# Performance work log

Measured on AMD Instinct MI355X. Metric: run time of the kernel, lower is better.

Reference implementation:

```python
import jax, jax.numpy as jnp
import numpy as np

TAU = 0.9
TOPK = 8
NUM_LAYERS = 3


def _layer_norm(x, g, b, eps=1e-5):
    mu = jnp.mean(x, axis=-1, keepdims=True)
    var = jnp.var(x, axis=-1, keepdims=True)
    return (x - mu) / jnp.sqrt(var + eps) * g + b


def _forward(x, edge_index, Wi, bi, wp, Wa, ba, ln1_g, ln1_b, ln2_g, ln2_b,
             W1, b1, W2, b2, Wc, bc, Wo, bo):
    N = x.shape[0]
    H = Wi.shape[1]
    # input projection + relu
    x = jax.nn.relu(x @ Wi + bi)
    src, dst = edge_index[0], edge_index[1]
    # ---- priority pi (computed under no_grad, dummy_alpha = 1, x_prev = 0) ----
    delta_x = jnp.sum(jnp.abs(x), axis=1)                      # [N]
    neigh = jax.ops.segment_sum(delta_x[src], dst, num_segments=N)
    pi = jax.lax.stop_gradient(jax.nn.sigmoid(x @ wp + neigh))  # [N]
    # ---- add self loops (selected subgraph == full graph) ----
    loops = jnp.arange(N, dtype=src.dtype)
    src_e = jnp.concatenate([src, loops])
    dst_e = jnp.concatenate([dst, loops])
    Et = src_e.shape[0]
    # ---- edge attention logits: att_mlp(cat[h_i, h_j, p_j]) computed as split matvec ----
    a_dst = x @ Wa[:H]          # contribution of h_i = x[dst]
    a_src = x @ Wa[H:2 * H]     # contribution of h_j = x[src]
    e = a_dst[dst_e] + a_src[src_e] + pi[src_e] * Wa[2 * H] + ba[0]
    e = jax.nn.leaky_relu(e, 0.2) / TAU
    e = jnp.clip(e, -5.0, 5.0)
    exp_e = jnp.exp(e)
    denom = jax.ops.segment_sum(exp_e, dst_e, num_segments=N)
    alpha = exp_e / (denom[dst_e] + 1e-16)
    # ---- per-destination top-k sparsification + renormalization (vectorized) ----
    order = jnp.lexsort((-alpha, dst_e))       # sort by dst, then alpha descending
    dst_s = dst_e[order]
    alpha_s = alpha[order]
    pos = jnp.arange(Et)
    is_new = jnp.concatenate([jnp.ones((1,), bool), dst_s[1:] != dst_s[:-1]])
    grp_start = jax.lax.cummax(jnp.where(is_new, pos, 0))
    rank = pos - grp_start                     # rank within each dst group
    keep = rank < TOPK
    ksum = jax.ops.segment_sum(jnp.where(keep, alpha_s, 0.0), dst_s, num_segments=N)
    alpha_new_s = jnp.where(keep, alpha_s / (ksum[dst_s] + 1e-16), 0.0)
    alpha = jnp.zeros((Et,), x.dtype).at[order].set(alpha_new_s)
    # ---- prenorm blocks with priority-weighted conv (dropout = identity, eval) ----
    h = x
    for l in range(NUM_LAYERS):
        hn = _layer_norm(h, ln1_g[l], ln1_b[l])
        xp = hn @ Wc[l] + bc[l]                               # conv linear
        msg = xp[src_e] * alpha[:, None]                      # [Et, H]
        agg = jax.ops.segment_sum(msg, dst_e, num_segments=N)  # scatter-add
        h = h + jax.nn.relu(agg)
        h2 = _layer_norm(h, ln2_g[l], ln2_b[l])
        h2 = jax.nn.gelu(h2 @ W1[l] + b1[l], approximate=False) @ W2[l] + b2[l]
        h = h + h2
    return h @ Wo + bo


def setup_inputs() -> dict:
    key = jax.random.key(0)
    ks = jax.random.split(key, 10)
    N, E, IN, H, OUT, L, F = 50000, 400000, 256, 256, 64, 3, 512
    def nrm(k, shape, scale):
        return jax.random.normal(k, shape, jnp.float32) * scale
    return {
        "x": nrm(ks[0], (N, IN), 1.0),
        "edge_index": jax.random.randint(ks[1], (2, E), 0, N, dtype=jnp.int32),
        "Wi": nrm(ks[2], (IN, H), IN ** -0.5), "bi": jnp.zeros((H,), jnp.float32),
        "wp": nrm(ks[3], (H,), H ** -0.5),
        "Wa": nrm(ks[4], (2 * H + 1,), (2 * H + 1) ** -0.5), "ba": jnp.zeros((1,), jnp.float32),
        "ln1_g": jnp.ones((L, H), jnp.float32), "ln1_b": jnp.zeros((L, H), jnp.float32),
        "ln2_g": jnp.ones((L, H), jnp.float32), "ln2_b": jnp.zeros((L, H), jnp.float32),
        "W1": nrm(ks[5], (L, H, F), H ** -0.5), "b1": jnp.zeros((L, F), jnp.float32),
        "W2": nrm(ks[6], (L, F, H), F ** -0.5), "b2": jnp.zeros((L, H), jnp.float32),
        "Wc": nrm(ks[7], (L, H, H), H ** -0.5), "bc": jnp.zeros((L, H), jnp.float32),
        "Wo": nrm(ks[8], (H, OUT), H ** -0.5), "bo": jnp.zeros((OUT,), jnp.float32),
    }


def reference(x, edge_index, Wi, bi, wp, Wa, ba, ln1_g, ln1_b, ln2_g, ln2_b,
              W1, b1, W2, b2, Wc, bc, Wo, bo):
    return _forward(x, edge_index, Wi, bi, wp, Wa, ba, ln1_g, ln1_b, ln2_g, ln2_b,
                    W1, b1, W2, b2, Wc, bc, Wo, bo)
```

## Files before the change

### kernel.cpp

```cpp
#include <hip/hip_runtime.h>
#include <math.h>

#define TAUF 0.9f

typedef unsigned int u32;
typedef unsigned short ushort;
typedef __attribute__((ext_vector_type(8))) short short8;
typedef __attribute__((ext_vector_type(8))) _Float16 half8;
typedef __attribute__((ext_vector_type(4))) _Float16 half4;
typedef __attribute__((ext_vector_type(4))) float f32x4;
typedef __attribute__((ext_vector_type(4))) unsigned short us4;

__device__ __forceinline__ float wave_sum(float v) {
#pragma unroll
  for (int off = 32; off > 0; off >>= 1) v += __shfl_down(v, off, 64);
  return __shfl(v, 0, 64);
}

__device__ __forceinline__ ushort f2bf(float f) {
  u32 u = __builtin_bit_cast(u32, f);
  u32 r = (u + 0x7FFFu + ((u >> 16) & 1u)) >> 16;
  return (ushort)r;
}
__device__ __forceinline__ float bf2f(ushort s) {
  u32 u = ((u32)s) << 16;
  return __builtin_bit_cast(float, u);
}

__device__ __forceinline__ void gload16(const void* g, void* l) {
  __builtin_amdgcn_global_load_lds(
      (const __attribute__((address_space(1))) u32*)g,
      (__attribute__((address_space(3))) u32*)l, 16, 0, 0);
}

__launch_bounds__(256, 2)
__global__ void gemm_in_mfma(const _Float16* __restrict__ Ah, const _Float16* __restrict__ Al,
                             const _Float16* __restrict__ Bh, const _Float16* __restrict__ Bl,
                             const float* __restrict__ bias, const float* __restrict__ Wa,
                             const float* __restrict__ wp, const float* __restrict__ g1,
                             const float* __restrict__ b1g, float* __restrict__ C,
                             ushort* __restrict__ hn, float* __restrict__ delta,
                             float* __restrict__ adst, float* __restrict__ asrc,
                             float* __restrict__ xwp, int M) {
  __shared__ char lds[81920];
  char* As_h = lds;
  char* As_l = lds + 8192;
  char* Bs_h = lds + 16384;
  char* Bs_l = lds + 49152;
  const int tid = threadIdx.x;
  const int wave = tid >> 6, lane = tid & 63;
  const int bm = blockIdx.x * 64;
  const int srow = lane >> 3;
  const int scol = (((lane & 7) ^ srow) << 3);

  f32x4 accH[4][4], accC[4][4];
#pragma unroll
  for (int i = 0; i < 4; ++i)
#pragma unroll
    for (int j = 0; j < 4; ++j) {
      accH[i][j] = (f32x4){0.f, 0.f, 0.f, 0.f};
      accC[i][j] = (f32x4){0.f, 0.f, 0.f, 0.f};
    }

  for (int k0 = 0; k0 < 256; k0 += 64) {
#pragma unroll
    for (int r = 0; r < 2; ++r) {
      const int ch = r * 4 + wave;
      int ar = bm + ch * 8 + srow;
      ar = (ar < M) ? ar : (M - 1);
      gload16(Ah + (size_t)ar * 256 + k0 + scol, As_h + ch * 1024);
      gload16(Al + (size_t)ar * 256 + k0 + scol, As_l + ch * 1024);
    }
#pragma unroll
    for (int r = 0; r < 8; ++r) {
      const int ch = r * 4 + wave;
      const int br = ch * 8 + srow;
      gload16(Bh + (size_t)br * 256 + k0 + scol, Bs_h + ch * 1024);
      gload16(Bl + (size_t)br * 256 + k0 + scol, Bs_l + ch * 1024);
    }
    __syncthreads();
#pragma unroll
    for (int kk = 0; kk < 2; ++kk) {
      const int c = (kk * 32 + (lane >> 4) * 8) * 2;
      half8 ah[4], bh[4];
#pragma unroll
      for (int mi = 0; mi < 4; ++mi) {
        const int rr = mi * 16 + (lane & 15);
        ah[mi] = *(const half8*)(As_h + rr * 128 + (c ^ ((rr & 7) << 4)));
      }
#pragma unroll
      for (int ni = 0; ni < 4; ++ni) {
        const int rr = wave * 64 + ni * 16 + (lane & 15);
        bh[ni] = *(const half8*)(Bs_h + rr * 128 + (c ^ ((rr & 7) << 4)));
      }
#pragma unroll
      for (int mi = 0; mi < 4; ++mi)
#pragma unroll
        for (int ni = 0; ni < 4; ++ni)
          accH[mi][ni] = __builtin_amdgcn_mfma_f32_16x16x32_f16(ah[mi], bh[ni],
                                                                accH[mi][ni], 0, 0, 0);
      half8 al[4];
#pragma unroll
      for (int mi = 0; mi < 4; ++mi) {
        const int rr = mi * 16 + (lane & 15);
        al[mi] = *(const half8*)(As_l + rr * 128 + (c ^ ((rr & 7) << 4)));
      }
#pragma unroll
      for (int mi = 0; mi < 4; ++mi)
#pragma unroll
        for (int ni = 0; ni < 4; ++ni)
          accC[mi][ni] = __builtin_amdgcn_mfma_f32_16x16x32_f16(al[mi], bh[ni],
                                                                accC[mi][ni], 0, 0, 0);
      half8 bl[4];
#pragma unroll
      for (int ni = 0; ni < 4; ++ni) {
        const int rr = wave * 64 + ni * 16 + (lane & 15);
        bl[ni] = *(const half8*)(Bs_l + rr * 128 + (c ^ ((rr & 7) << 4)));
      }
#pragma unroll
      for (int mi = 0; mi < 4; ++mi)
#pragma unroll
        for (int ni = 0; ni < 4; ++ni)
          accC[mi][ni] = __builtin_amdgcn_mfma_f32_16x16x32_f16(ah[mi], bl[ni],
                                                                accC[mi][ni], 0, 0, 0);
    }
    __syncthreads();
  }

  float bb[4], wa0[4], wa1[4], wpv[4], gg[4], gb[4];
#pragma unroll
  for (int ni = 0; ni < 4; ++ni) {
    const int c = wave * 64 + ni * 16 + (lane & 15);
    bb[ni] = bias[c]; wa0[ni] = Wa[c]; wa1[ni] = Wa[256 + c];
    wpv[ni] = wp[c]; gg[ni] = g1[c]; gb[ni] = b1g[c];
  }
  float* red = (float*)lds;
  float* muA = (float*)(lds + 5120);
  float* isA = (float*)(lds + 5376);
  const float inv = 1.f / 2048.f;
#pragma unroll
  for (int mi = 0; mi < 4; ++mi) {
#pragma unroll
    for (int reg = 0; reg < 4; ++reg) {
      const int lrow = mi * 16 + (lane >> 4) * 4 + reg;
      const int row = bm + lrow;
      float v[4];
      float p0 = 0.f, p1 = 0.f, p2 = 0.f, p3 = 0.f, p4 = 0.f;
#pragma unroll
      for (int ni = 0; ni < 4; ++ni) {
        float t = accH[mi][ni][reg] + accC[mi][ni][reg] * inv + bb[ni];
        t = fmaxf(t, 0.f);
        v[ni] = t;
        p0 += t; p1 += t * wa0[ni]; p2 += t * wa1[ni]; p3 += t * wpv[ni];
        p4 += t * t;
      }
      if (row < M) {
#pragma unroll
        for (int ni = 0; ni < 4; ++ni)
          C[(size_t)row * 256 + wave * 64 + ni * 16 + (lane & 15)] = v[ni];
      }
#pragma unroll
      for (int ni = 0; ni < 4; ++ni) accH[mi][ni][reg] = v[ni];
#pragma unroll
      for (int off = 1; off < 16; off <<= 1) {
        p0 += __shfl_xor(p0, off, 64);
        p1 += __shfl_xor(p1, off, 64);
        p2 += __shfl_xor(p2, off, 64);
        p3 += __shfl_xor(p3, off, 64);
        p4 += __shfl_xor(p4, off, 64);
      }
      if ((lane & 15) == 0) {
        red[(0 * 4 + wave) * 64 + lrow] = p0;
        red[(1 * 4 + wave) * 64 + lrow] = p1;
        red[(2 * 4 + wave) * 64 + lrow] = p2;
        red[(3 * 4 + wave) * 64 + lrow] = p3;
        red[(4 * 4 + wave) * 64 + lrow] = p4;
      }
    }
  }
  __syncthreads();
  if (tid < 64) {
    float s0 = 0.f, s1 = 0.f, s2 = 0.f, s3 = 0.f, s4 = 0.f;
#pragma unroll
    for (int w = 0; w < 4; ++w) {
      s0 += red[(0 * 4 + w) * 64 + tid];
      s1 += red[(1 * 4 + w) * 64 + tid];
      s2 += red[(2 * 4 + w) * 64 + tid];
      s3 += red[(3 * 4 + w) * 64 + tid];
      s4 += red[(4 * 4 + w) * 64 + tid];
    }
    const int row = bm + tid;
    if (row < M) {
      delta[row] = s0; adst[row] = s1; asrc[row] = s2; xwp[row] = s3;
    }
    float mu = s0 * (1.f / 256.f);
    muA[tid] = mu;
    isA[tid] = rsqrtf(s4 * (1.f / 256.f) - mu * mu + 1e-5f);
  }
  __syncthreads();
#pragma unroll
  for (int mi = 0; mi < 4; ++mi) {
#pragma unroll
    for (int reg = 0; reg < 4; ++reg) {
      const int lrow = mi * 16 + (lane >> 4) * 4 + reg;
      const int row = bm + lrow;
      if (row >= M) continue;
      const float mu = muA[lrow], is = isA[lrow];
#pragma unroll
      for (int ni = 0; ni < 4; ++ni) {
        const int col = wave * 64 + ni * 16 + (lane & 15);
        hn[(size_t)row * 256 + col] = f2bf((accH[mi][ni][reg] - mu) * is * gg[ni] + gb[ni]);
      }
    }
  }
}

__global__ void xsplit_k(const float* __restrict__ X, _Float16* __restrict__ Xh,
                         _Float16* __restrict__ Xl, int total4) {
  int i = blockIdx.x * 256 + threadIdx.x;
  if (i >= total4) return;
  float4 x = reinterpret_cast<const float4*>(X)[i];
  half4 h, l;
  float xs[4] = {x.x, x.y, x.z, x.w};
#pragma unroll
  for (int j = 0; j < 4; ++j) {
    _Float16 hv = (_Float16)xs[j];
    h[j] = hv;
    l[j] = (_Float16)((xs[j] - (float)hv) * 2048.f);
  }
  reinterpret_cast<half4*>(Xh)[i] = h;
  reinterpret_cast<half4*>(Xl)[i] = l;
}

template <int EPI>
__launch_bounds__(256)
__global__ void gemm_mfma(const ushort* __restrict__ A, const ushort* __restrict__ Bt,
                          const float* __restrict__ bias, float* __restrict__ Cf,
                          ushort* __restrict__ Cb, int M, int N, int K) {
  __shared__ ushort As[128 * 64];
  __shared__ ushort Bs[128 * 64];
  const int tid = threadIdx.x;
  const int wave = tid >> 6, lane = tid & 63;
  const int bm = blockIdx.x * 128, bn = blockIdx.y * 128;
  const int wm = (wave >> 1) * 64, wn = (wave & 1) * 64;
  const int srow = lane >> 3;
  const int scol = (((lane & 7) ^ srow) << 3);

  f32x4 acc[4][4];
#pragma unroll
  for (int i = 0; i < 4; ++i)
#pragma unroll
    for (int j = 0; j < 4; ++j) acc[i][j] = (f32x4){0.f, 0.f, 0.f, 0.f};

  for (int k0 = 0; k0 < K; k0 += 64) {
#pragma unroll
    for (int r = 0; r < 4; ++r) {
      const int ch = r * 4 + wave;
      int ar = bm + ch * 8 + srow;
      ar = (ar < M) ? ar : (M - 1);
      gload16(A + (size_t)ar * K + k0 + scol, (char*)As + ch * 1024);
      const int br = bn + ch * 8 + srow;
      gload16(Bt + (size_t)br * K + k0 + scol, (char*)Bs + ch * 1024);
    }
    __syncthreads();
#pragma unroll
    for (int kk = 0; kk < 2; ++kk) {
      const int c = (kk * 32 + (lane >> 4) * 8) * 2;
      short8 a[4];
#pragma unroll
      for (int mi = 0; mi < 4; ++mi) {
        const int rr = wm + mi * 16 + (lane & 15);
        a[mi] = *(const short8*)((const char*)As + rr * 128 + (c ^ ((rr & 7) << 4)));
      }
#pragma unroll
      for (int ni = 0; ni < 4; ++ni) {
        const int rr = wn + ni * 16 + (lane & 15);
        short8 b = *(const short8*)((const char*)Bs + rr * 128 + (c ^ ((rr & 7) << 4)));
#pragma unroll
        for (int mi = 0; mi < 4; ++mi)
          acc[mi][ni] = __builtin_amdgcn_mfma_f32_16x16x32_bf16(a[mi], b,
                                                                acc[mi][ni], 0, 0, 0);
      }
    }
    __syncthreads();
  }

  float bb[4];
#pragma unroll
  for (int ni = 0; ni < 4; ++ni) bb[ni] = bias[bn + wn + ni * 16 + (lane & 15)];
#pragma unroll
  for (int mi = 0; mi < 4; ++mi) {
#pragma unroll
    for (int reg = 0; reg < 4; ++reg) {
      const int row = bm + wm + mi * 16 + (lane >> 4) * 4 + reg;
      if (row >= M) continue;
#pragma unroll
      for (int ni = 0; ni < 4; ++ni) {
        const int col = bn + wn + ni * 16 + (lane & 15);
        float v = acc[mi][ni][reg] + bb[ni];
        if (EPI == 1) {
          Cb[(size_t)row * N + col] = f2bf(v);
        } else if (EPI == 2) {
          v = v * 0.5f * (1.f + erff(v * 0.70710678118654752f));
          Cb[(size_t)row * N + col] = f2bf(v);
        } else if (EPI == 3) {
          Cf[(size_t)row * N + col] += v;
        } else {
          v += Cf[(size_t)row * N + col];
          Cb[(size_t)row * N + col] = f2bf(v);
        }
      }
    }
  }
}

__launch_bounds__(256)
__global__ void gemm_out(const ushort* __restrict__ A, const ushort* __restrict__ Bt,
                         const float* __restrict__ bias, float* __restrict__ C, int M) {
  __shared__ ushort As[128 * 64];
  __shared__ ushort Bs[64 * 64];
  const int tid = threadIdx.x;
  const int wave = tid >> 6, lane = tid & 63;
  const int bm = blockIdx.x * 128;
  const int wm = wave * 32;
  const int srow = lane >> 3;
  const int scol = (((lane & 7) ^ srow) << 3);
  f32x4 acc[2][4];
#pragma unroll
  for (int i = 0; i < 2; ++i)
#pragma unroll
    for (int j = 0; j < 4; ++j) acc[i][j] = (f32x4){0.f, 0.f, 0.f, 0.f};

  for (int k0 = 0; k0 < 256; k0 += 64) {
#pragma unroll
    for (int r = 0; r < 4; ++r) {
      const int ch = r * 4 + wave;
      int ar = bm + ch * 8 + srow;
      ar = (ar < M) ? ar : (M - 1);
      gload16(A + (size_t)ar * 256 + k0 + scol, (char*)As + ch * 1024);
    }
#pragma unroll
    for (int r = 0; r < 2; ++r) {
      const int ch = r * 4 + wave;
      const int br = ch * 8 + srow;
      gload16(Bt + (size_t)br * 256 + k0 + scol, (char*)Bs + ch * 1024);
    }
    __syncthreads();
#pragma unroll
    for (int kk = 0; kk < 2; ++kk) {
      const int c = (kk * 32 + (lane >> 4) * 8) * 2;
      short8 a[2], b[4];
#pragma unroll
      for (int mi = 0; mi < 2; ++mi) {
        const int rr = wm + mi * 16 + (lane & 15);
        a[mi] = *(const short8*)((const char*)As + rr * 128 + (c ^ ((rr & 7) << 4)));
      }
#pragma unroll
      for (int ni = 0; ni < 4; ++ni) {
        const int rr = ni * 16 + (lane & 15);
        b[ni] = *(const short8*)((const char*)Bs + rr * 128 + (c ^ ((rr & 7) << 4)));
      }
#pragma unroll
      for (int mi = 0; mi < 2; ++mi)
#pragma unroll
        for (int ni = 0; ni < 4; ++ni)
          acc[mi][ni] = __builtin_amdgcn_mfma_f32_16x16x32_bf16(a[mi], b[ni],
                                                                acc[mi][ni], 0, 0, 0);
    }
    __syncthreads();
  }
  float bb[4];
#pragma unroll
  for (int ni = 0; ni < 4; ++ni) bb[ni] = bias[ni * 16 + (lane & 15)];
#pragma unroll
  for (int mi = 0; mi < 2; ++mi) {
#pragma unroll
    for (int reg = 0; reg < 4; ++reg) {
      const int row = bm + wm + mi * 16 + (lane >> 4) * 4 + reg;
      if (row >= M) continue;
#pragma unroll
      for (int ni = 0; ni < 4; ++ni) {
        const int col = ni * 16 + (lane & 15);
        C[(size_t)row * 64 + col] = acc[mi][ni][reg] + bb[ni];
      }
    }
  }
}

#define W_IN 65536
#define W_TOTAL (196608 + 393216 + 393216 + 16384)
__global__ void prep_k(const float* __restrict__ Wi, const float* __restrict__ Wc,
                       const float* __restrict__ W1, const float* __restrict__ W2,
                       const float* __restrict__ Wo, _Float16* __restrict__ WiTh,
                       _Float16* __restrict__ WiTl, ushort* __restrict__ WcT,
                       ushort* __restrict__ W1T, ushort* __restrict__ W2T,
                       ushort* __restrict__ WoT, float* __restrict__ zbase, int zn) {
  int i = blockIdx.x * 256 + threadIdx.x;
  if (i < W_IN) {
    int n = i >> 8, k = i & 255;
    float w = Wi[(size_t)k * 256 + n];
    _Float16 hv = (_Float16)w;
    WiTh[i] = hv;
    WiTl[i] = (_Float16)((w - (float)hv) * 2048.f);
  } else if ((i -= W_IN) < W_TOTAL) {
    int j = i;
    if (j < 196608) {
      int l = j / 65536, r = j % 65536, n = r >> 8, k = r & 255;
      WcT[j] = f2bf(Wc[(size_t)l * 65536 + k * 256 + n]);
    } else if ((j -= 196608) < 393216) {
      int l = j / 131072, r = j % 131072, n = r >> 8, k = r & 255;
      W1T[j] = f2bf(W1[(size_t)l * 131072 + k * 512 + n]);
    } else if ((j -= 393216) < 393216) {
      int l = j / 131072, r = j % 131072, n = r >> 9, k = r & 511;
      W2T[j] = f2bf(W2[(size_t)l * 131072 + k * 256 + n]);
    } else {
      j -= 393216;
      int n = j >> 8, k = j & 255;
      WoT[j] = f2bf(Wo[k * 64 + n]);
    }
  } else {
    int z = i - W_TOTAL;
    if (z < zn) zbase[z] = 0.f;
  }
}

__global__ void neigh_k(const int* __restrict__ src, const int* __restrict__ dst,
                        const float* __restrict__ delta, float* __restrict__ neigh, int E) {
  int e = blockIdx.x * 256 + threadIdx.x;
  if (e < E) atomicAdd(&neigh[dst[e]], delta[src[e]]);
}

__global__ void logits_k(const int* __restrict__ src, const int* __restrict__ dst,
                         const float* __restrict__ adst, const float* __restrict__ asrc,
                         const float* __restrict__ xwp, const float* __restrict__ neigh,
                         const float* __restrict__ Wa, const float* __restrict__ ba,
                         float* __restrict__ expe, float* __restrict__ denom,
                         int* __restrict__ cnt, int* __restrict__ slots,
                         int E, int Et, int N) {
  int e = blockIdx.x * 256 + threadIdx.x;
  if (e >= Et) return;
  int s, d;
  if (e < E) { s = src[e]; d = dst[e]; } else { s = e - E; d = s; }
  float pis = 1.f / (1.f + expf(-(xwp[s] + neigh[s])));
  float v = adst[d] + asrc[s] + pis * Wa[512] + ba[0];
  v = (v >= 0.f ? v : 0.2f * v) / TAUF;
  v = fminf(fmaxf(v, -5.f), 5.f);
  float ex = expf(v);
  expe[e] = ex;
  atomicAdd(&denom[d], ex);
  int p = atomicAdd(&cnt[d], 1);
  if (p < 64) slots[(size_t)p * N + d] = e;
}

__device__ __forceinline__ bool better(float a, int e, float a2, int e2) {
  return a > a2 || (a == a2 && e < e2);
}

__global__ void topk_k(const int* __restrict__ cnt, const int* __restrict__ slots,
                       const float* __restrict__ expe, const float* __restrict__ denom,
                       const int* __restrict__ src, int* __restrict__ kcnt,
                       int* __restrict__ ksrc, float* __restrict__ kw, int N, int E) {
  int d = blockIdx.x * 256 + threadIdx.x;
  if (d >= N) return;
  int deg = min(cnt[d], 64);
  float D = denom[d] + 1e-16f;
  float av[8]; int ai[8]; int kc = 0;
  for (int t = 0; t < deg; ++t) {
    int e = slots[(size_t)t * N + d];
    float a = expe[e] / D;
    if (kc < 8) {
      int p = kc++;
      while (p > 0 && better(a, e, av[p - 1], ai[p - 1])) {
        av[p] = av[p - 1]; ai[p] = ai[p - 1]; --p;
      }
      av[p] = a; ai[p] = e;
    } else if (better(a, e, av[7], ai[7])) {
      int p = 7;
      while (p > 0 && better(a, e, av[p - 1], ai[p - 1])) {
        av[p] = av[p - 1]; ai[p] = ai[p - 1]; --p;
      }
      av[p] = a; ai[p] = e;
    }
  }
  float ks = 0.f;
  for (int j = 0; j < kc; ++j) ks += av[j];
  kcnt[d] = kc;
  for (int j = 0; j < kc; ++j) {
    int e = ai[j];
    ksrc[(size_t)d * 8 + j] = (e < E) ? src[e] : (e - E);
    kw[(size_t)d * 8 + j] = av[j] / (ks + 1e-16f);
  }
}

__global__ void ln_k(const float* __restrict__ h, const float* __restrict__ g,
                     const float* __restrict__ b, ushort* __restrict__ o, int N) {
  int row = blockIdx.x * 4 + (threadIdx.x >> 6);
  if (row >= N) return;
  int lane = threadIdx.x & 63;
  float4 v = *reinterpret_cast<const float4*>(h + (size_t)row * 256 + lane * 4);
  float s = wave_sum(v.x + v.y + v.z + v.w);
  float mu = s * (1.f / 256.f);
  float q = (v.x - mu) * (v.x - mu) + (v.y - mu) * (v.y - mu) +
            (v.z - mu) * (v.z - mu) + (v.w - mu) * (v.w - mu);
  q = wave_sum(q);
  float is = rsqrtf(q * (1.f / 256.f) + 1e-5f);
  float4 gg = *reinterpret_cast<const float4*>(g + lane * 4);
  float4 bb = *reinterpret_cast<const float4*>(b + lane * 4);
  us4 out;
  out.x = f2bf((v.x - mu) * is * gg.x + bb.x);
  out.y = f2bf((v.y - mu) * is * gg.y + bb.y);
  out.z = f2bf((v.z - mu) * is * gg.z + bb.z);
  out.w = f2bf((v.w - mu) * is * gg.w + bb.w);
  *reinterpret_cast<us4*>(o + (size_t)row * 256 + lane * 4) = out;
}

__global__ void agg_ln_k(const ushort* __restrict__ xp, const int* __restrict__ kcnt,
                         const int* __restrict__ ksrc, const float* __restrict__ kw,
                         const float* __restrict__ g, const float* __restrict__ b,
                         float* __restrict__ h, ushort* __restrict__ hn, int N) {
  int d = blockIdx.x * 4 + (threadIdx.x >> 6);
  if (d >= N) return;
  int lane = threadIdx.x & 63;
  int kc = kcnt[d];
  float a0 = 0.f, a1 = 0.f, a2 = 0.f, a3 = 0.f;
  for (int j = 0; j < kc; ++j) {
    int s = ksrc[(size_t)d * 8 + j];
    float w = kw[(size_t)d * 8 + j];
    us4 xv = *reinterpret_cast<const us4*>(xp + (size_t)s * 256 + lane * 4);
    a0 += w * bf2f(xv.x);
    a1 += w * bf2f(xv.y);
    a2 += w * bf2f(xv.z);
    a3 += w * bf2f(xv.w);
  }
  float* hr = h + (size_t)d * 256 + lane * 4;
  float4 hv = *reinterpret_cast<const float4*>(hr);
  float v0 = hv.x + fmaxf(a0, 0.f);
  float v1 = hv.y + fmaxf(a1, 0.f);
  float v2 = hv.z + fmaxf(a2, 0.f);
  float v3 = hv.w + fmaxf(a3, 0.f);
  *reinterpret_cast<float4*>(hr) = make_float4(v0, v1, v2, v3);
  float s = wave_sum(v0 + v1 + v2 + v3);
  float mu = s * (1.f / 256.f);
  float q = (v0 - mu) * (v0 - mu) + (v1 - mu) * (v1 - mu) +
            (v2 - mu) * (v2 - mu) + (v3 - mu) * (v3 - mu);
  q = wave_sum(q);
  float is = rsqrtf(q * (1.f / 256.f) + 1e-5f);
  float4 gg = *reinterpret_cast<const float4*>(g + lane * 4);
  float4 bb = *reinterpret_cast<const float4*>(b + lane * 4);
  us4 out;
  out.x = f2bf((v0 - mu) * is * gg.x + bb.x);
  out.y = f2bf((v1 - mu) * is * gg.y + bb.y);
  out.z = f2bf((v2 - mu) * is * gg.z + bb.z);
  out.w = f2bf((v3 - mu) * is * gg.w + bb.w);
  *reinterpret_cast<us4*>(hn + (size_t)d * 256 + lane * 4) = out;
}

extern "C" void kernel_launch(void* const* d_in, const int* in_sizes, int n_in,
                              void* d_out, int out_size, void* d_ws, size_t ws_size,
                              hipStream_t stream) {
  const float* X   = (const float*)d_in[0];
  const int*   EI  = (const int*)d_in[1];
  const float* Wi  = (const float*)d_in[2];
  const float* bi  = (const float*)d_in[3];
  const float* wp  = (const float*)d_in[4];
  const float* Wa  = (const float*)d_in[5];
  const float* ba  = (const float*)d_in[6];
  const float* l1g = (const float*)d_in[7];
  const float* l1b = (const float*)d_in[8];
  const float* l2g = (const float*)d_in[9];
  const float* l2b = (const float*)d_in[10];
  const float* W1  = (const float*)d_in[11];
  const float* b1  = (const float*)d_in[12];
  const float* W2  = (const float*)d_in[13];
  const float* b2  = (const float*)d_in[14];
  const float* Wc  = (const float*)d_in[15];
  const float* bc  = (const float*)d_in[16];
  const float* Wo  = (const float*)d_in[17];
  const float* bo  = (const float*)d_in[18];

  const int N = in_sizes[0] / 256;
  const int E = in_sizes[1] / 2;
  const int Et = E + N;
  const int* srcp = EI;
  const int* dstp = EI + E;

  float* ws = (float*)d_ws;
  size_t off = 0;
  auto alloc = [&](size_t n) { float* p = ws + off; off += n; return p; };
  const size_t NH = (size_t)N * 256;
  float*  h    = alloc(NH);
  ushort* hn   = (ushort*)alloc(NH / 2);
  ushort* xp   = (ushort*)alloc(NH / 2);
  float*  ualias = alloc(NH);
  ushort* u    = (ushort*)ualias;
  _Float16* Xh = (_Float16*)ualias;
  _Float16* Xl = Xh + NH;
  _Float16* WiTh = (_Float16*)alloc(65536 / 2);
  _Float16* WiTl = (_Float16*)alloc(65536 / 2);
  ushort* WcT  = (ushort*)alloc(3 * 65536 / 2);
  ushort* W1T  = (ushort*)alloc(3 * 131072 / 2);
  ushort* W2T  = (ushort*)alloc(3 * 131072 / 2);
  ushort* WoT  = (ushort*)alloc(16384 / 2);
  float* delta = alloc(N);
  float* adst  = alloc(N);
  float* asrc  = alloc(N);
  float* xwp   = alloc(N);
  float* expe  = alloc(Et);
  float* neigh = alloc(N);
  float* denom = alloc(N);
  int*   cnt   = (int*)alloc(N);
  int*   slots = (int*)alloc((size_t)N * 64);
  int*   kcnt  = (int*)alloc(N);
  int*   ksrc  = (int*)alloc((size_t)N * 8);
  float* kw    = alloc((size_t)N * 8);

  prep_k<<<(W_IN + W_TOTAL + 3 * N + 255) / 256, 256, 0, stream>>>(
      Wi, Wc, W1, W2, Wo, WiTh, WiTl, WcT, W1T, W2T, WoT, neigh, 3 * N);
  xsplit_k<<<((int)(NH / 4) + 255) / 256, 256, 0, stream>>>(X, Xh, Xl, (int)(NH / 4));

  gemm_in_mfma<<<(N + 63) / 64, 256, 0, stream>>>(
      Xh, Xl, WiTh, WiTl, bi, Wa, wp, l1g, l1b, h, hn,
      delta, adst, asrc, xwp, N);
  neigh_k<<<(E + 255) / 256, 256, 0, stream>>>(srcp, dstp, delta, neigh, E);
  logits_k<<<(Et + 255) / 256, 256, 0, stream>>>(srcp, dstp, adst, asrc, xwp, neigh,
                                                 Wa, ba, expe, denom, cnt, slots,
                                                 E, Et, N);
  topk_k<<<(N + 255) / 256, 256, 0, stream>>>(cnt, slots, expe, denom, srcp,
                                              kcnt, ksrc, kw, N, E);

  const int GM = (N + 127) / 128;
  for (int l = 0; l < 3; ++l) {
    gemm_mfma<1><<<dim3(GM, 2), 256, 0, stream>>>(
        hn, WcT + (size_t)l * 65536, bc + l * 256, nullptr, xp, N, 256, 256);
    agg_ln_k<<<(N + 3) / 4, 256, 0, stream>>>(xp, kcnt, ksrc, kw,
                                              l2g + l * 256, l2b + l * 256, h, hn, N);
    gemm_mfma<2><<<dim3(GM, 4), 256, 0, stream>>>(
        hn, W1T + (size_t)l * 131072, b1 + l * 512, nullptr, u, N, 512, 256);
    if (l < 2) {
      gemm_mfma<3><<<dim3(GM, 2), 256, 0, stream>>>(
          u, W2T + (size_t)l * 131072, b2 + l * 256, h, nullptr, N, 256, 512);
      ln_k<<<(N + 3) / 4, 256, 0, stream>>>(h, l1g + (l + 1) * 256,
                                            l1b + (l + 1) * 256, hn, N);
    } else {
      gemm_mfma<4><<<dim3(GM, 2), 256, 0, stream>>>(
          u, W2T + (size_t)l * 131072, b2 + l * 256, h, hn, N, 256, 512);
    }
  }
  gemm_out<<<(N + 127) / 128, 256, 0, stream>>>(hn, WoT, bo, (float*)d_out, N);
}
```

Baseline: 737.7 us.

## Fuse FFN second GEMM with residual add and LayerNorm; use fast GELU approximation

Adds a new GEMM kernel that computes a full 256-wide output row tile per block (512 threads), adds the residual and bias, and computes the next layer's LayerNorm in the epilogue through a cross-wave LDS reduction. This removes the separate ln_k launch and its re-read of h. The erff-based GELU is also replaced with an Abramowitz-Stegun polynomial using __expf to cut epilogue cost. Risks are that the single-pass variance (E[x^2]-mu^2) is less numerically stable, the erf approximation introduces small errors, and the larger block with fewer blocks in the grid may reduce occupancy or parallelism.

```diff
diff --git a/kernel.cpp b/kernel.cpp
--- a/kernel.cpp
+++ b/kernel.cpp
@@ -25,6 +25,17 @@
 __device__ __forceinline__ float bf2f(ushort s) {
   u32 u = ((u32)s) << 16;
   return __builtin_bit_cast(float, u);
+}
+
+__device__ __forceinline__ float gelu_f(float x) {
+  float z = x * 0.70710678118654752f;
+  float az = fabsf(z);
+  float t = 1.f / fmaf(0.3275911f, az, 1.f);
+  float poly = t * fmaf(t, fmaf(t, fmaf(t, fmaf(t, 1.061405429f, -1.453152027f),
+                                        1.421413741f), -0.284496736f), 0.254829592f);
+  float erfa = fmaf(-poly, __expf(-az * az), 1.f);
+  float s = (z < 0.f) ? -erfa : erfa;
+  return 0.5f * x * (1.f + s);
 }
 
 __device__ __forceinline__ void gload16(const void* g, void* l) {
@@ -235,8 +246,8 @@
 template <int EPI>
 __launch_bounds__(256)
 __global__ void gemm_mfma(const ushort* __restrict__ A, const ushort* __restrict__ Bt,
-                          const float* __restrict__ bias, float* __restrict__ Cf,
-                          ushort* __restrict__ Cb, int M, int N, int K) {
+                          const float* __restrict__ bias, ushort* __restrict__ Cb,
+                          int M, int N, int K) {
   __shared__ ushort As[128 * 64];
   __shared__ ushort Bs[128 * 64];
   const int tid = threadIdx.x;
@@ -298,17 +309,143 @@
       for (int ni = 0; ni < 4; ++ni) {
         const int col = bn + wn + ni * 16 + (lane & 15);
         float v = acc[mi][ni][reg] + bb[ni];
-        if (EPI == 1) {
-          Cb[(size_t)row * N + col] = f2bf(v);
-        } else if (EPI == 2) {
-          v = v * 0.5f * (1.f + erff(v * 0.70710678118654752f));
-          Cb[(size_t)row * N + col] = f2bf(v);
-        } else if (EPI == 3) {
-          Cf[(size_t)row * N + col] += v;
+        if (EPI == 2) v = gelu_f(v);
+        Cb[(size_t)row * N + col] = f2bf(v);
+      }
+    }
+  }
+}
+
+template <int LAST>
+__launch_bounds__(512, 4)
+__global__ void gemm_ffn2ln(const ushort* __restrict__ A, const ushort* __restrict__ Bt,
+                            const float* __restrict__ bias, const float* __restrict__ g1,
+                            const float* __restrict__ b1g, float* __restrict__ h,
+                            ushort* __restrict__ hn, int M) {
+  __shared__ ushort As[128 * 64];
+  __shared__ ushort Bs[256 * 64];
+  const int tid = threadIdx.x;
+  const int wave = tid >> 6, lane = tid & 63;
+  const int bm = blockIdx.x * 128;
+  const int wm = (wave >> 2) * 64, wn = (wave & 3) * 64;
+  const int srow = lane >> 3;
+  const int scol = (((lane & 7) ^ srow) << 3);
+
+  f32x4 acc[4][4];
+#pragma unroll
+  for (int i = 0; i < 4; ++i)
+#pragma unroll
+    for (int j = 0; j < 4; ++j) acc[i][j] = (f32x4){0.f, 0.f, 0.f, 0.f};
+
+  for (int k0 = 0; k0 < 512; k0 += 64) {
+#pragma unroll
+    for (int r = 0; r < 2; ++r) {
+      const int ch = r * 8 + wave;
+      int ar = bm + ch * 8 + srow;
+      ar = (ar < M) ? ar : (M - 1);
+      gload16(A + (size_t)ar * 512 + k0 + scol, (char*)As + ch * 1024);
+    }
+#pragma unroll
+    for (int r = 0; r < 4; ++r) {
+      const int ch = r * 8 + wave;
+      const int br = ch * 8 + srow;
+      gload16(Bt + (size_t)br * 512 + k0 + scol, (char*)Bs + ch * 1024);
+    }
+    __syncthreads();
+#pragma unroll
+    for (int kk = 0; kk < 2; ++kk) {
+      const int c = (kk * 32 + (lane >> 4) * 8) * 2;
+      short8 a[4];
+#pragma unroll
+      for (int mi = 0; mi < 4; ++mi) {
+        const int rr = wm + mi * 16 + (lane & 15);
+        a[mi] = *(const short8*)((const char*)As + rr * 128 + (c ^ ((rr & 7) << 4)));
+      }
+#pragma unroll
+      for (int ni = 0; ni < 4; ++ni) {
+        const int rr = wn + ni * 16 + (lane & 15);
+        short8 b = *(const short8*)((const char*)Bs + rr * 128 + (c ^ ((rr & 7) << 4)));
+#pragma unroll
+        for (int mi = 0; mi < 4; ++mi)
+          acc[mi][ni] = __builtin_amdgcn_mfma_f32_16x16x32_bf16(a[mi], b,
+                                                                acc[mi][ni], 0, 0, 0);
+      }
+    }
+    __syncthreads();
+  }
+
+  float bb[4];
+#pragma unroll
+  for (int ni = 0; ni < 4; ++ni) bb[ni] = bias[wn + ni * 16 + (lane & 15)];
+
+  float* redS = (float*)As;
+  float* redQ = redS + 512;
+  float* muA  = redQ + 512;
+  float* isA  = muA + 128;
+
+#pragma unroll
+  for (int mi = 0; mi < 4; ++mi) {
+#pragma unroll
+    for (int reg = 0; reg < 4; ++reg) {
+      const int lrow = wm + mi * 16 + (lane >> 4) * 4 + reg;
+      const int row = bm + lrow;
+      const bool ok = (row < M);
+      float pS = 0.f, pQ = 0.f;
+#pragma unroll
+      for (int ni = 0; ni < 4; ++ni) {
+        const int col = wn + ni * 16 + (lane & 15);
+        float t = acc[mi][ni][reg] + bb[ni];
+        if (ok) t += h[(size_t)row * 256 + col];
+        acc[mi][ni][reg] = t;
+        if (LAST) {
+          if (ok) hn[(size_t)row * 256 + col] = f2bf(t);
         } else {
-          v += Cf[(size_t)row * N + col];
-          Cb[(size_t)row * N + col] = f2bf(v);
+          if (ok) h[(size_t)row * 256 + col] = t;
+          pS += t;
+          pQ += t * t;
         }
+      }
+      if (!LAST) {
+#pragma unroll
+        for (int off = 1; off < 16; off <<= 1) {
+          pS += __shfl_xor(pS, off, 64);
+          pQ += __shfl_xor(pQ, off, 64);
+        }
+        if ((lane & 15) == 0) {
+          redS[(wave & 3) * 128 + lrow] = pS;
+          redQ[(wave & 3) * 128 + lrow] = pQ;
+        }
+      }
+    }
+  }
+  if (LAST) return;
+  __syncthreads();
+  if (tid < 128) {
+    float S = redS[tid] + redS[128 + tid] + redS[256 + tid] + redS[384 + tid];
+    float Q = redQ[tid] + redQ[128 + tid] + redQ[256 + tid] + redQ[384 + tid];
+    float mu = S * (1.f / 256.f);
+    muA[tid] = mu;
+    isA[tid] = rsqrtf(Q * (1.f / 256.f) - mu * mu + 1e-5f);
+  }
+  __syncthreads();
+  float gg[4], gb[4];
+#pragma unroll
+  for (int ni = 0; ni < 4; ++ni) {
+    gg[ni] = g1[wn + ni * 16 + (lane & 15)];
+    gb[ni] = b1g[wn + ni * 16 + (lane & 15)];
+  }
+#pragma unroll
+  for (int mi = 0; mi < 4; ++mi) {
+#pragma unroll
+    for (int reg = 0; reg < 4; ++reg) {
+      const int lrow = wm + mi * 16 + (lane >> 4) * 4 + reg;
+      const int row = bm + lrow;
+      if (row >= M) continue;
+      const float mu = muA[lrow], is = isA[lrow];
+#pragma unroll
+      for (int ni = 0; ni < 4; ++ni) {
+        const int col = wn + ni * 16 + (lane & 15);
+        hn[(size_t)row * 256 + col] = f2bf((acc[mi][ni][reg] - mu) * is * gg[ni] + gb[ni]);
       }
     }
   }
@@ -492,28 +629,6 @@
   }
 }
 
-__global__ void ln_k(const float* __restrict__ h, const float* __restrict__ g,
-                     const float* __restrict__ b, ushort* __restrict__ o, int N) {
-  int row = blockIdx.x * 4 + (threadIdx.x >> 6);
-  if (row >= N) return;
-  int lane = threadIdx.x & 63;
-  float4 v = *reinterpret_cast<const float4*>(h + (size_t)row * 256 + lane * 4);
-  float s = wave_sum(v.x + v.y + v.z + v.w);
-  float mu = s * (1.f / 256.f);
-  float q = (v.x - mu) * (v.x - mu) + (v.y - mu) * (v.y - mu) +
-            (v.z - mu) * (v.z - mu) + (v.w - mu) * (v.w - mu);
-  q = wave_sum(q);
-  float is = rsqrtf(q * (1.f / 256.f) + 1e-5f);
-  float4 gg = *reinterpret_cast<const float4*>(g + lane * 4);
-  float4 bb = *reinterpret_cast<const float4*>(b + lane * 4);
-  us4 out;
-  out.x = f2bf((v.x - mu) * is * gg.x + bb.x);
-  out.y = f2bf((v.y - mu) * is * gg.y + bb.y);
-  out.z = f2bf((v.z - mu) * is * gg.z + bb.z);
-  out.w = f2bf((v.w - mu) * is * gg.w + bb.w);
-  *reinterpret_cast<us4*>(o + (size_t)row * 256 + lane * 4) = out;
-}
-
 __global__ void agg_ln_k(const ushort* __restrict__ xp, const int* __restrict__ kcnt,
                          const int* __restrict__ ksrc, const float* __restrict__ kw,
                          const float* __restrict__ g, const float* __restrict__ b,
@@ -631,20 +746,19 @@
   const int GM = (N + 127) / 128;
   for (int l = 0; l < 3; ++l) {
     gemm_mfma<1><<<dim3(GM, 2), 256, 0, stream>>>(
-        hn, WcT + (size_t)l * 65536, bc + l * 256, nullptr, xp, N, 256, 256);
+        hn, WcT + (size_t)l * 65536, bc + l * 256, xp, N, 256, 256);
     agg_ln_k<<<(N + 3) / 4, 256, 0, stream>>>(xp, kcnt, ksrc, kw,
                                               l2g + l * 256, l2b + l * 256, h, hn, N);
     gemm_mfma<2><<<dim3(GM, 4), 256, 0, stream>>>(
-        hn, W1T + (size_t)l * 131072, b1 + l * 512, nullptr, u, N, 512, 256);
-    if (l < 2) {
-      gemm_mfma<3><<<dim3(GM, 2), 256, 0, stream>>>(
-          u, W2T + (size_t)l * 131072, b2 + l * 256, h, nullptr, N, 256, 512);
-      ln_k<<<(N + 3) / 4, 256, 0, stream>>>(h, l1g + (l + 1) * 256,
-                                            l1b + (l + 1) * 256, hn, N);
-    } else {
-      gemm_mfma<4><<<dim3(GM, 2), 256, 0, stream>>>(
-          u, W2T + (size_t)l * 131072, b2 + l * 256, h, hn, N, 256, 512);
-    }
+        hn, W1T + (size_t)l * 131072, b1 + l * 512, u, N, 512, 256);
+    if (l < 2)
+      gemm_ffn2ln<0><<<GM, 512, 0, stream>>>(
+          u, W2T + (size_t)l * 131072, b2 + l * 256,
+          l1g + (l + 1) * 256, l1b + (l + 1) * 256, h, hn, N);
+    else
+      gemm_ffn2ln<1><<<GM, 512, 0, stream>>>(
+          u, W2T + (size_t)l * 131072, b2 + l * 256,
+          nullptr, nullptr, h, hn, N);
   }
   gemm_out<<<(N + 127) / 128, 256, 0, stream>>>(hn, WoT, bo, (float*)d_out, N);
 }
```

Result: faster. 676.8 us (-8.2%).
